# Performance work log

Measured on AMD Instinct MI355X. Metric: run time of the kernel, lower is better.

## Reference

```python
import jax, jax.numpy as jnp
import numpy as np


def _cayley():
    """8x8x8 structure constants of Cl(3,0): (a*b)[r] = sum_pq a[p] b[q] C[p,q,r].
    Built by evaluating the original geometric_product formulas on basis one-hots."""
    C = np.zeros((8, 8, 8), dtype=np.float32)
    for p in range(8):
        a = np.zeros(8, dtype=np.float32); a[p] = 1.0
        for q in range(8):
            b = np.zeros(8, dtype=np.float32); b[q] = 1.0
            C[p, q] = [
                a[0]*b[0] + a[1]*b[1] + a[2]*b[2] + a[3]*b[3] - a[4]*b[4] - a[5]*b[5] - a[6]*b[6] - a[7]*b[7],
                a[0]*b[1] + a[1]*b[0] - a[2]*b[4] - a[3]*b[5] + a[4]*b[2] + a[5]*b[3] - a[6]*b[7] - a[7]*b[6],
                a[0]*b[2] + a[1]*b[4] + a[2]*b[0] - a[3]*b[6] - a[4]*b[1] + a[5]*b[7] + a[6]*b[3] + a[7]*b[5],
                a[0]*b[3] + a[1]*b[5] + a[2]*b[6] + a[3]*b[0] - a[4]*b[7] - a[5]*b[1] - a[6]*b[2] - a[7]*b[4],
                a[0]*b[4] + a[1]*b[2] - a[2]*b[1] + a[3]*b[7] + a[4]*b[0] - a[5]*b[6] + a[6]*b[5] + a[7]*b[3],
                a[0]*b[5] + a[1]*b[3] - a[2]*b[7] - a[3]*b[1] + a[4]*b[6] + a[5]*b[0] - a[6]*b[4] - a[7]*b[2],
                a[0]*b[6] + a[1]*b[7] + a[2]*b[3] - a[3]*b[2] - a[4]*b[5] + a[5]*b[4] + a[6]*b[0] + a[7]*b[1],
                a[0]*b[7] + a[1]*b[6] - a[2]*b[5] + a[3]*b[4] + a[4]*b[3] - a[5]*b[2] + a[6]*b[1] + a[7]*b[0],
            ]
    return C

_C = jnp.asarray(_cayley())  # [8,8,8]

BATCH, IN_F, OUT_F = 4096, 512, 512


def setup_inputs() -> dict:
    key = jax.random.key(0)
    k1, k2, k3 = jax.random.split(key, 3)
    return {
        "x": jax.random.normal(k1, (BATCH, IN_F, 8), dtype=jnp.float32),
        "weight": jax.random.normal(k2, (OUT_F, IN_F, 8), dtype=jnp.float32),
        "bias": jax.random.normal(k3, (OUT_F, 8), dtype=jnp.float32),
    }


def reference(x, weight, bias):
    # Precontract weight with Cayley table: Wc[i,j,p,r] = sum_q weight[i,j,q] C[p,q,r]
    Wc = jnp.einsum('ijq,pqr->ijpr', weight, _C)
    # out[b,i,r] = sum_{j,p} x[b,j,p] Wc[i,j,p,r]  (one big GEMM) + bias
    out = jnp.einsum('bjp,ijpr->bir', x, Wc) + bias[None, :, :]
    return out
```

## Files before the change

### kernel.cpp

```cpp
#include <hip/hip_runtime.h>
#include <hip/hip_bf16.h>


#define MDIM 4096
#define NDIM 4096
#define KDIM 4096
#define KTILES 64

typedef __attribute__((ext_vector_type(8))) __bf16 bf16x8;
typedef __attribute__((ext_vector_type(4))) float f32x4;
typedef __attribute__((ext_vector_type(8))) unsigned short ushort8;

__device__ __forceinline__ unsigned short f2bf(float f) {
  unsigned int u = __builtin_bit_cast(unsigned int, f);
  u += 0x7fffu + ((u >> 16) & 1u);
  return (unsigned short)(u >> 16);
}

static constexpr int QTAB[8][8] = {
  {0,1,2,3,4,5,6,7},
  {1,0,4,5,2,3,7,6},
  {2,4,0,6,1,7,3,5},
  {3,5,6,0,7,1,2,4},
  {4,2,1,7,0,6,5,3},
  {5,3,7,1,6,0,4,2},
  {6,7,3,2,5,4,0,1},
  {7,6,5,4,3,2,1,0},
};
static constexpr unsigned short SBIT[8][8] = {
  {0,0,0,0,0x8000,0x8000,0x8000,0x8000},
  {0,0,0x8000,0x8000,0,0,0x8000,0x8000},
  {0,0,0,0x8000,0x8000,0,0,0},
  {0,0,0,0,0x8000,0x8000,0x8000,0x8000},
  {0,0,0x8000,0,0,0x8000,0,0},
  {0,0,0x8000,0x8000,0,0,0x8000,0x8000},
  {0,0,0,0x8000,0x8000,0,0,0},
  {0,0,0x8000,0,0,0x8000,0,0},
};

__global__ __launch_bounds__(256) void cast_x_kernel(
    const float* __restrict__ X, unsigned short* __restrict__ Xb) {
  const size_t t = (size_t)blockIdx.x * 256 + threadIdx.x;
  const float4* p = (const float4*)(X + t * 8);
  float4 a = p[0], b = p[1];
  ushort8 o;
  o[0] = f2bf(a.x); o[1] = f2bf(a.y); o[2] = f2bf(a.z); o[3] = f2bf(a.w);
  o[4] = f2bf(b.x); o[5] = f2bf(b.y); o[6] = f2bf(b.z); o[7] = f2bf(b.w);
  *(ushort8*)(Xb + t * 8) = o;
}

__global__ __launch_bounds__(256) void build_wc_kernel(
    const float* __restrict__ W, unsigned short* __restrict__ Wb) {
  const int t = blockIdx.x * 256 + threadIdx.x;
  const int i = t >> 9;
  const int j = t & 511;
  const float4 w0 = *(const float4*)(W + (size_t)t * 8);
  const float4 w1 = *(const float4*)(W + (size_t)t * 8 + 4);
  const unsigned short b[8] = {f2bf(w0.x), f2bf(w0.y), f2bf(w0.z), f2bf(w0.w),
                               f2bf(w1.x), f2bf(w1.y), f2bf(w1.z), f2bf(w1.w)};
#pragma unroll
  for (int r = 0; r < 8; ++r) {
    ushort8 o;
#pragma unroll
    for (int p = 0; p < 8; ++p)
      o[p] = (unsigned short)(b[QTAB[r][p]] ^ SBIT[r][p]);
    *(ushort8*)(Wb + (size_t)(i * 8 + r) * KDIM + j * 8) = o;
  }
}

typedef const __attribute__((address_space(1))) unsigned int as1_uint;
typedef __attribute__((address_space(3))) unsigned int as3_uint;

__device__ __forceinline__ void gload_lds16(const unsigned short* g,
                                            unsigned short* l) {
  __builtin_amdgcn_global_load_lds((as1_uint*)g, (as3_uint*)l, 16, 0, 0);
}

__device__ __forceinline__ void stage_half(
    const unsigned short* __restrict__ G, int gbase_row, int tile, int kh,
    unsigned short* lds_slot, int wid, int lane) {
  const int colswz = ((lane & 3) ^ ((lane >> 3) & 3)) * 8;
#pragma unroll
  for (int q = 0; q < 2; ++q) {
    const int c = wid * 2 + q;
    const unsigned short* src = G
        + (size_t)(gbase_row + c * 16 + (lane >> 2)) * KDIM
        + tile * 64 + kh * 32 + colswz;
    gload_lds16(src, lds_slot + c * 512);
  }
}

#define BAR()  asm volatile("s_barrier" ::: "memory")
#define VM6()  asm volatile("s_waitcnt vmcnt(6)" ::: "memory")
#define VM0()  asm volatile("s_waitcnt vmcnt(0)" ::: "memory")
#define NOSTAGE (void)0

#define PH(bufb, kk, mh, RDB, STAGE_STMT, VMC_STMT) do {                      \
    const unsigned short* As_ = &lds[(bufb)*4 + (kk)][0];                     \
    const unsigned short* Bs_ = &lds[(bufb)*4 + 2 + (kk)][0];                 \
    bf16x8 af[4];                                                             \
    _Pragma("unroll") for (int mi = 0; mi < 4; ++mi)                          \
      af[mi] = *(const bf16x8*)(As_ + (wm*128 + ((mh)*4+mi)*16 + fr)*32 + fqs*8); \
    if (RDB) {                                                                \
      _Pragma("unroll") for (int n = 0; n < 4; ++n)                           \
        bfr[n] = *(const bf16x8*)(Bs_ + (wn*64 + n*16 + fr)*32 + fqs*8);      \
    }                                                                         \
    STAGE_STMT;                                                               \
    VMC_STMT;                                                                 \
    BAR();                                                                    \
    __builtin_amdgcn_s_setprio(1);                                            \
    _Pragma("unroll") for (int mi = 0; mi < 4; ++mi)                          \
      _Pragma("unroll") for (int n = 0; n < 4; ++n)                           \
        acc[(mh)*4+mi][n] = __builtin_amdgcn_mfma_f32_16x16x32_bf16(          \
            af[mi], bfr[n], acc[(mh)*4+mi][n], 0, 0, 0);                      \
    __builtin_amdgcn_s_setprio(0);                                            \
    BAR();                                                                    \
  } while (0)

__global__ __launch_bounds__(512, 2) void gemm_bt_bias(
    const unsigned short* __restrict__ A,
    const unsigned short* __restrict__ B,
    const float* __restrict__ bias,
    float* __restrict__ C) {
  __shared__ unsigned short lds[8][8192];

  const int tid = threadIdx.x;
  const int wid = tid >> 6;
  const int lane = tid & 63;
  const int wm = wid >> 2;
  const int wn = wid & 3;
  const int fr = lane & 15;
  const int fq = lane >> 4;
  const int fqs = fq ^ ((fr >> 1) & 3);

  const int raw = blockIdx.x;
  const int wg = (raw & 7) * 32 + (raw >> 3);
  const int brow = (wg >> 4) * 256;
  const int bcol = (wg & 15) * 256;

  f32x4 acc[8][4];
#pragma unroll
  for (int m = 0; m < 8; ++m)
#pragma unroll
    for (int n = 0; n < 4; ++n) acc[m][n] = (f32x4){0.f, 0.f, 0.f, 0.f};
  bf16x8 bfr[4];

  stage_half(A, brow, 0, 0, &lds[0][0], wid, lane);
  stage_half(A, brow, 0, 1, &lds[1][0], wid, lane);
  stage_half(B, bcol, 0, 0, &lds[2][0], wid, lane);
  stage_half(B, bcol, 0, 1, &lds[3][0], wid, lane);
  stage_half(A, brow, 1, 0, &lds[4][0], wid, lane);
  stage_half(B, bcol, 1, 0, &lds[6][0], wid, lane);
  stage_half(B, bcol, 1, 1, &lds[7][0], wid, lane);
  VM6();
  BAR();

  for (int i = 0; i < KTILES / 2 - 1; ++i) {
    const int t0 = 2 * i, t1 = 2 * i + 1;
    PH(0, 0, 0, 1, stage_half(A, brow, t1,     1, &lds[5][0], wid, lane), NOSTAGE);
    PH(0, 0, 1, 0, stage_half(B, bcol, t0 + 2, 0, &lds[2][0], wid, lane), NOSTAGE);
    PH(0, 1, 0, 1, stage_half(A, brow, t0 + 2, 0, &lds[0][0], wid, lane), NOSTAGE);
    PH(0, 1, 1, 0, stage_half(B, bcol, t0 + 2, 1, &lds[3][0], wid, lane), VM6());
    PH(1, 0, 0, 1, stage_half(A, brow, t0 + 2, 1, &lds[1][0], wid, lane), NOSTAGE);
    PH(1, 0, 1, 0, stage_half(B, bcol, t1 + 2, 0, &lds[6][0], wid, lane), NOSTAGE);
    PH(1, 1, 0, 1, stage_half(A, brow, t1 + 2, 0, &lds[4][0], wid, lane), NOSTAGE);
    PH(1, 1, 1, 0, stage_half(B, bcol, t1 + 2, 1, &lds[7][0], wid, lane), VM6());
  }

  PH(0, 0, 0, 1, stage_half(A, brow, KTILES - 1, 1, &lds[5][0], wid, lane), NOSTAGE);
  PH(0, 0, 1, 0, NOSTAGE, NOSTAGE);
  PH(0, 1, 0, 1, NOSTAGE, NOSTAGE);
  PH(0, 1, 1, 0, NOSTAGE, VM0());
  PH(1, 0, 0, 1, NOSTAGE, NOSTAGE);
  PH(1, 0, 1, 0, NOSTAGE, NOSTAGE);
  PH(1, 1, 0, 1, NOSTAGE, NOSTAGE);
  PH(1, 1, 1, 0, NOSTAGE, NOSTAGE);

#pragma unroll
  for (int n = 0; n < 4; ++n) {
    const int col = bcol + wn * 64 + n * 16 + fr;
    const float bvs = bias[col];
#pragma unroll
    for (int m = 0; m < 8; ++m) {
      const int row0 = brow + wm * 128 + m * 16 + fq * 4;
#pragma unroll
      for (int j = 0; j < 4; ++j)
        C[(size_t)(row0 + j) * NDIM + col] = acc[m][n][j] + bvs;
    }
  }
}

extern "C" void kernel_launch(void* const* d_in, const int* in_sizes, int n_in,
                              void* d_out, int out_size, void* d_ws, size_t ws_size,
                              hipStream_t stream) {
  const float* x = (const float*)d_in[0];
  const float* w = (const float*)d_in[1];
  const float* bias = (const float*)d_in[2];
  float* out = (float*)d_out;

  unsigned short* Xb = (unsigned short*)d_ws;
  unsigned short* Wb = Xb + (size_t)MDIM * KDIM;

  cast_x_kernel<<<8192, 256, 0, stream>>>(x, Xb);
  build_wc_kernel<<<1024, 256, 0, stream>>>(w, Wb);
  gemm_bt_bias<<<256, 512, 0, stream>>>(Xb, Wb, bias, out);
}
```

Measured before the change: 245.6 us.

## Software-pipeline LDS fragment reads with double-buffered registers across MFMA phases

The GEMM main loop is restructured so each phase issues LDS reads for the next phase's A and B fragments before running the current phase's 16 MFMAs. Two register sets per operand (afA/afB, bU/bV) alternate between phases. The goal is to hide LDS read latency behind matrix-core work instead of waiting on each phase's reads before its MFMAs. In exchange it needs more live VGPRs on top of the large accumulator set, which risks spills or lower occupancy under the 512x2 launch bounds.

```diff
diff --git a/kernel.cpp b/kernel.cpp
--- a/kernel.cpp
+++ b/kernel.cpp
@@ -93,28 +93,25 @@
 #define BAR()  asm volatile("s_barrier" ::: "memory")
 #define VM6()  asm volatile("s_waitcnt vmcnt(6)" ::: "memory")
 #define VM0()  asm volatile("s_waitcnt vmcnt(0)" ::: "memory")
-#define NOSTAGE (void)0
-
-#define PH(bufb, kk, mh, RDB, STAGE_STMT, VMC_STMT) do {                      \
-    const unsigned short* As_ = &lds[(bufb)*4 + (kk)][0];                     \
-    const unsigned short* Bs_ = &lds[(bufb)*4 + 2 + (kk)][0];                 \
-    bf16x8 af[4];                                                             \
-    _Pragma("unroll") for (int mi = 0; mi < 4; ++mi)                          \
-      af[mi] = *(const bf16x8*)(As_ + (wm*128 + ((mh)*4+mi)*16 + fr)*32 + fqs*8); \
-    if (RDB) {                                                                \
-      _Pragma("unroll") for (int n = 0; n < 4; ++n)                           \
-        bfr[n] = *(const bf16x8*)(Bs_ + (wn*64 + n*16 + fr)*32 + fqs*8);      \
+
+#define RDA(dst, bufb, kk, mh) do {                                           \
+    _Pragma("unroll") for (int mi_ = 0; mi_ < 4; ++mi_)                       \
+      dst[mi_] = *(const bf16x8*)(&lds[(bufb)*4 + (kk)][0]                    \
+          + ((wm)*128 + ((mh)*4 + mi_)*16 + fr)*32 + fqs*8);                  \
+  } while (0)
+#define RDB_(dst, bufb, kk) do {                                              \
+    _Pragma("unroll") for (int ni_ = 0; ni_ < 4; ++ni_)                       \
+      dst[ni_] = *(const bf16x8*)(&lds[(bufb)*4 + 2 + (kk)][0]                \
+          + ((wn)*64 + ni_*16 + fr)*32 + fqs*8);                              \
+  } while (0)
+#define MFMA16(afv, bv, mh) do {                                              \
+    __builtin_amdgcn_s_setprio(1);                                            \
+    _Pragma("unroll") for (int mi_ = 0; mi_ < 4; ++mi_) {                     \
+      _Pragma("unroll") for (int ni_ = 0; ni_ < 4; ++ni_)                     \
+        acc[(mh)*4 + mi_][ni_] = __builtin_amdgcn_mfma_f32_16x16x32_bf16(     \
+            afv[mi_], bv[ni_], acc[(mh)*4 + mi_][ni_], 0, 0, 0);              \
     }                                                                         \
-    STAGE_STMT;                                                               \
-    VMC_STMT;                                                                 \
-    BAR();                                                                    \
-    __builtin_amdgcn_s_setprio(1);                                            \
-    _Pragma("unroll") for (int mi = 0; mi < 4; ++mi)                          \
-      _Pragma("unroll") for (int n = 0; n < 4; ++n)                           \
-        acc[(mh)*4+mi][n] = __builtin_amdgcn_mfma_f32_16x16x32_bf16(          \
-            af[mi], bfr[n], acc[(mh)*4+mi][n], 0, 0, 0);                      \
     __builtin_amdgcn_s_setprio(0);                                            \
-    BAR();                                                                    \
   } while (0)
 
 __global__ __launch_bounds__(512, 2) void gemm_bt_bias(
@@ -143,7 +140,7 @@
   for (int m = 0; m < 8; ++m)
 #pragma unroll
     for (int n = 0; n < 4; ++n) acc[m][n] = (f32x4){0.f, 0.f, 0.f, 0.f};
-  bf16x8 bfr[4];
+  bf16x8 afA[4], afB[4], bU[4], bV[4];
 
   stage_half(A, brow, 0, 0, &lds[0][0], wid, lane);
   stage_half(A, brow, 0, 1, &lds[1][0], wid, lane);
@@ -154,27 +151,41 @@
   stage_half(B, bcol, 1, 1, &lds[7][0], wid, lane);
   VM6();
   BAR();
+  RDA(afA, 0, 0, 0);
+  RDB_(bU, 0, 0);
 
   for (int i = 0; i < KTILES / 2 - 1; ++i) {
     const int t0 = 2 * i, t1 = 2 * i + 1;
-    PH(0, 0, 0, 1, stage_half(A, brow, t1,     1, &lds[5][0], wid, lane), NOSTAGE);
-    PH(0, 0, 1, 0, stage_half(B, bcol, t0 + 2, 0, &lds[2][0], wid, lane), NOSTAGE);
-    PH(0, 1, 0, 1, stage_half(A, brow, t0 + 2, 0, &lds[0][0], wid, lane), NOSTAGE);
-    PH(0, 1, 1, 0, stage_half(B, bcol, t0 + 2, 1, &lds[3][0], wid, lane), VM6());
-    PH(1, 0, 0, 1, stage_half(A, brow, t0 + 2, 1, &lds[1][0], wid, lane), NOSTAGE);
-    PH(1, 0, 1, 0, stage_half(B, bcol, t1 + 2, 0, &lds[6][0], wid, lane), NOSTAGE);
-    PH(1, 1, 0, 1, stage_half(A, brow, t1 + 2, 0, &lds[4][0], wid, lane), NOSTAGE);
-    PH(1, 1, 1, 0, stage_half(B, bcol, t1 + 2, 1, &lds[7][0], wid, lane), VM6());
-  }
-
-  PH(0, 0, 0, 1, stage_half(A, brow, KTILES - 1, 1, &lds[5][0], wid, lane), NOSTAGE);
-  PH(0, 0, 1, 0, NOSTAGE, NOSTAGE);
-  PH(0, 1, 0, 1, NOSTAGE, NOSTAGE);
-  PH(0, 1, 1, 0, NOSTAGE, VM0());
-  PH(1, 0, 0, 1, NOSTAGE, NOSTAGE);
-  PH(1, 0, 1, 0, NOSTAGE, NOSTAGE);
-  PH(1, 1, 0, 1, NOSTAGE, NOSTAGE);
-  PH(1, 1, 1, 0, NOSTAGE, NOSTAGE);
+    stage_half(A, brow, t1, 1, &lds[5][0], wid, lane);
+    BAR(); RDA(afB, 0, 0, 1);                  MFMA16(afA, bU, 0); BAR();
+    stage_half(B, bcol, t0 + 2, 0, &lds[2][0], wid, lane);
+    BAR(); RDA(afA, 0, 1, 0); RDB_(bV, 0, 1);  MFMA16(afB, bU, 1); BAR();
+    stage_half(A, brow, t0 + 2, 0, &lds[0][0], wid, lane);
+    BAR(); RDA(afB, 0, 1, 1);                  MFMA16(afA, bV, 0); BAR();
+    stage_half(B, bcol, t0 + 2, 1, &lds[3][0], wid, lane);
+    VM6();
+    BAR(); RDA(afA, 1, 0, 0); RDB_(bU, 1, 0);  MFMA16(afB, bV, 1); BAR();
+    stage_half(A, brow, t0 + 2, 1, &lds[1][0], wid, lane);
+    BAR(); RDA(afB, 1, 0, 1);                  MFMA16(afA, bU, 0); BAR();
+    stage_half(B, bcol, t1 + 2, 0, &lds[6][0], wid, lane);
+    BAR(); RDA(afA, 1, 1, 0); RDB_(bV, 1, 1);  MFMA16(afB, bU, 1); BAR();
+    stage_half(A, brow, t1 + 2, 0, &lds[4][0], wid, lane);
+    BAR(); RDA(afB, 1, 1, 1);                  MFMA16(afA, bV, 0); BAR();
+    stage_half(B, bcol, t1 + 2, 1, &lds[7][0], wid, lane);
+    VM6();
+    BAR(); RDA(afA, 0, 0, 0); RDB_(bU, 0, 0);  MFMA16(afB, bV, 1); BAR();
+  }
+
+  stage_half(A, brow, KTILES - 1, 1, &lds[5][0], wid, lane);
+  BAR(); RDA(afB, 0, 0, 1);                  MFMA16(afA, bU, 0); BAR();
+  BAR(); RDA(afA, 0, 1, 0); RDB_(bV, 0, 1);  MFMA16(afB, bU, 1); BAR();
+  BAR(); RDA(afB, 0, 1, 1);                  MFMA16(afA, bV, 0); BAR();
+  VM0();
+  BAR(); RDA(afA, 1, 0, 0); RDB_(bU, 1, 0);  MFMA16(afB, bV, 1); BAR();
+  BAR(); RDA(afB, 1, 0, 1);                  MFMA16(afA, bU, 0); BAR();
+  BAR(); RDA(afA, 1, 1, 0); RDB_(bV, 1, 1);  MFMA16(afB, bU, 1); BAR();
+  BAR(); RDA(afB, 1, 1, 1);                  MFMA16(afA, bV, 0); BAR();
+  BAR();                                     MFMA16(afB, bV, 1); BAR();
 
 #pragma unroll
   for (int n = 0; n < 4; ++n) {
```

After: 250.8 us. 2.1% more time.
